# Optimization experiments

Measured on AMD Instinct MI355X. Metric: run time of the kernel, lower is better.

The kernel has to match this reference:

```python
import jax, jax.numpy as jnp
import numpy as np

EPS = 1e-5

def _bn(x, gamma, beta):
    # training-mode BatchNorm1d over (batch, points) per channel; x: [B, C, N]
    mean = x.mean(axis=(0, 2), keepdims=True)
    var = x.var(axis=(0, 2), keepdims=True)
    return gamma[None, :, None] * (x - mean) * jax.lax.rsqrt(var + EPS) + beta[None, :, None]

def _conv_nn(x, idx, W, b):
    # x: [B, Cin, N_in]; idx: [N_out, k]; W: [Cout, Cin, k]
    g = x[:, :, idx]  # gather -> [B, Cin, N_out, k]
    return jnp.einsum('bink,oik->bon', g, W) + b[None, :, None]

def setup_inputs() -> dict:
    key = jax.random.key(0)
    ks = jax.random.split(key, 8)
    B, Cin, Cout = 32, 32, 64
    Nin, Nout, K, KP = 32768, 8192, 9, 4
    s = 0.05
    return {
        'x': jax.random.normal(ks[0], (B, Cin, Nin), jnp.float32),
        'W1': jax.random.normal(ks[1], (Cout, Cin, K), jnp.float32) * s,
        'b1': jnp.zeros((Cout,), jnp.float32),
        'W2': jax.random.normal(ks[2], (Cout, Cout, K), jnp.float32) * s,
        'b2': jnp.zeros((Cout,), jnp.float32),
        'We': jax.random.normal(ks[3], (Cout, Cin), jnp.float32) * s,
        'be': jnp.zeros((Cout,), jnp.float32),
        'g1': jnp.ones((Cout,), jnp.float32), 'beta1': jnp.zeros((Cout,), jnp.float32),
        'g2': jnp.ones((Cout,), jnp.float32), 'beta2': jnp.zeros((Cout,), jnp.float32),
        'g3': jnp.ones((Cout,), jnp.float32), 'beta3': jnp.zeros((Cout,), jnp.float32),
        'idx1': jax.random.randint(ks[4], (Nout, K), 0, Nin, jnp.int32),
        'idx2': jax.random.randint(ks[5], (Nout, K), 0, Nout, jnp.int32),
        'pool_idx': jax.random.randint(ks[6], (Nout, KP), 0, Nin, jnp.int32),
    }

def reference(x, W1, b1, W2, b2, We, be, g1, beta1, g2, beta2, g3, beta3, idx1, idx2, pool_idx):
    # main branch: ConvNN -> BN -> ReLU -> ConvNN -> BN
    out = jax.nn.relu(_bn(_conv_nn(x, idx1, W1, b1), g1, beta1))
    out = _bn(_conv_nn(out, idx2, W2, b2), g2, beta2)
    # shortcut: AvgPoolNN (k=4) -> 1x1 conv expand -> BN
    pooled = x[:, :, pool_idx].mean(axis=-1)  # [B, Cin, N_out]
    identity = _bn(jnp.einsum('bin,oi->bon', pooled, We) + be[None, :, None], g3, beta3)
    return jax.nn.relu(out + identity)
```

## Files before the change

### kernel.cpp

```cpp
#include <hip/hip_runtime.h>
#include <hip/hip_bf16.h>

typedef __attribute__((ext_vector_type(8))) short short8_t;
typedef __attribute__((ext_vector_type(4))) float f32x4_t;

#define NOUT 8192
#define NIN 32768
#define MTOT 262144.0f
#define ST_STRIPES 64

#define MF(a,b,c) __builtin_amdgcn_mfma_f32_16x16x32_bf16((a),(b),(c),0,0,0)

static __device__ __forceinline__ float bf2f(ushort u) {
    union { float f; unsigned int i; } x; x.i = ((unsigned int)u) << 16; return x.f;
}
static __device__ __forceinline__ ushort f2bfx(float f) {
    union { __hip_bfloat16 h; ushort u; } v;
    v.h = __float2bfloat16(f);
    return v.u;
}
static __device__ __forceinline__ short8_t i4s8(int4 v) {
    union { int4 i; short8_t s; } u; u.i = v; return u.s;
}

__global__ __launch_bounds__(256) void transpose_x_kernel(
    const float* __restrict__ x, ushort* __restrict__ xt)
{
    __shared__ ushort T[64][66];
    const int tid = threadIdx.x;
    const int n0 = blockIdx.x * 64, c0 = blockIdx.y * 64;
    const int lane64 = tid & 63, rb = (tid >> 6) * 16;
    #pragma unroll
    for (int r = 0; r < 16; ++r) {
        int c_l = rb + r;
        T[c_l][lane64] = f2bfx(x[(size_t)(c0 + c_l) * NIN + n0 + lane64]);
    }
    __syncthreads();
    #pragma unroll
    for (int r = 0; r < 16; ++r) {
        int n_l = rb + r;
        xt[(size_t)(n0 + n_l) * 1024 + c0 + lane64] = T[lane64][n_l];
    }
}

__global__ __launch_bounds__(256) void prep_w_kernel(
    const float* __restrict__ W1, const float* __restrict__ W2,
    const float* __restrict__ We,
    ushort* __restrict__ w1p, ushort* __restrict__ w2p, ushort* __restrict__ wep,
    float* __restrict__ stz)
{
    int t = blockIdx.x * 256 + threadIdx.x;
    const int N1 = 18432, N2 = 36864, N3 = 2048;
    if (t < 3 * ST_STRIPES * 128) stz[t] = 0.f;
    if (t < N1) {
        int e = t & 7, o = (t >> 3) & 63, seg = t >> 9;
        int fcg = seg & 3, k = seg >> 2;
        int i = fcg * 8 + e;
        w1p[t] = f2bfx(W1[o * 288 + i * 9 + k]);
    } else if (t < N1 + N2) {
        int t2 = t - N1;
        int e = t2 & 7, o = (t2 >> 3) & 63, seg = t2 >> 9;
        int fcg = seg & 3, kk = (seg >> 2) & 1, k = seg >> 3;
        int ci = kk * 32 + fcg * 8 + e;
        w2p[t2] = f2bfx(W2[o * 576 + ci * 9 + k]);
    } else if (t < N1 + N2 + N3) {
        int t3 = t - N1 - N2;
        wep[t3] = f2bfx(We[t3]);
    }
}

__global__ __launch_bounds__(512) void conv1_kernel(
    const ushort* __restrict__ xt, const int* __restrict__ idx1,
    const ushort* __restrict__ w1p, ushort* __restrict__ out1,
    float* __restrict__ st)
{
    __shared__ __align__(16) ushort Wl[18432];
    __shared__ float Ls[128];
    const int tid = threadIdx.x;
    const int lane = tid & 63, wv = tid >> 6;
    const int n = __builtin_amdgcn_readfirstlane(blockIdx.x * 8 + wv);
    const int l15 = lane & 15, fcg = lane >> 4, fc = fcg * 8;

    for (int i = tid; i < 2304; i += 512)
        ((int4*)Wl)[i] = ((const int4*)w1p)[i];
    if (tid < 128) Ls[tid] = 0.f;

    int rows[9];
    {
        const int* idxn = idx1 + n * 9;
        #pragma unroll
        for (int t = 0; t < 9; ++t) rows[t] = idxn[t];
    }
    __syncthreads();

    f32x4_t acc[2][4];
    #pragma unroll
    for (int m = 0; m < 2; ++m)
        #pragma unroll
        for (int nt = 0; nt < 4; ++nt) acc[m][nt] = (f32x4_t){0.f, 0.f, 0.f, 0.f};

    int4 A0[2], A1[2];

#define C1_PRE(K, A) { \
    const ushort* rp = xt + (size_t)rows[K] * 1024 + l15 * 32 + fc; \
    A[0] = *(const int4*)rp;           \
    A[1] = *(const int4*)(rp + 512);   }

#define C1_BODY(K, A) { \
    const ushort* wp = Wl + ((K) * 4 + fcg) * 512; \
    short8_t b0 = *(const short8_t*)(wp + l15 * 8); \
    short8_t b1 = *(const short8_t*)(wp + (16 + l15) * 8); \
    short8_t b2 = *(const short8_t*)(wp + (32 + l15) * 8); \
    short8_t b3 = *(const short8_t*)(wp + (48 + l15) * 8); \
    short8_t af0 = i4s8(A[0]), af1 = i4s8(A[1]); \
    acc[0][0] = MF(af0, b0, acc[0][0]); acc[1][0] = MF(af1, b0, acc[1][0]); \
    acc[0][1] = MF(af0, b1, acc[0][1]); acc[1][1] = MF(af1, b1, acc[1][1]); \
    acc[0][2] = MF(af0, b2, acc[0][2]); acc[1][2] = MF(af1, b2, acc[1][2]); \
    acc[0][3] = MF(af0, b3, acc[0][3]); acc[1][3] = MF(af1, b3, acc[1][3]); }

    C1_PRE(0, A0);
    #pragma unroll
    for (int t = 0; t < 4; ++t) {
        C1_PRE(2 * t + 1, A1);
        C1_BODY(2 * t, A0);
        C1_PRE(2 * t + 2, A0);
        C1_BODY(2 * t + 1, A1);
    }
    C1_BODY(8, A0);
#undef C1_PRE
#undef C1_BODY

    const size_t outbase = (size_t)n * 2048;
    #pragma unroll
    for (int m = 0; m < 2; ++m)
        #pragma unroll
        for (int nt = 0; nt < 4; ++nt)
            #pragma unroll
            for (int j = 0; j < 4; ++j) {
                int b = m * 16 + (lane >> 4) * 4 + j;
                int o = nt * 16 + l15;
                out1[outbase + b * 64 + o] = f2bfx(acc[m][nt][j]);
            }
    #pragma unroll
    for (int nt = 0; nt < 4; ++nt) {
        float s = 0.f, q = 0.f;
        #pragma unroll
        for (int m = 0; m < 2; ++m)
            #pragma unroll
            for (int j = 0; j < 4; ++j) { float v = acc[m][nt][j]; s += v; q += v * v; }
        s += __shfl_xor(s, 16); s += __shfl_xor(s, 32);
        q += __shfl_xor(q, 16); q += __shfl_xor(q, 32);
        if (lane < 16) {
            atomicAdd(&Ls[nt * 16 + lane], s);
            atomicAdd(&Ls[64 + nt * 16 + lane], q);
        }
    }
    __syncthreads();
    if (tid < 128) atomicAdd(&st[(blockIdx.x & (ST_STRIPES - 1)) * 128 + tid], Ls[tid]);
}

__global__ __launch_bounds__(256) void bn_relu_ip_kernel(
    ushort* __restrict__ buf, const float* __restrict__ ac)
{
    const int tid = threadIdx.x;
    const int o0 = (tid * 8) & 63;
    float a[8], c[8];
    #pragma unroll
    for (int e = 0; e < 8; ++e) { a[e] = ac[o0 + e]; c[e] = ac[64 + o0 + e]; }
    size_t base = (size_t)(blockIdx.x * 256 + tid) * 8;
    const size_t stride = (size_t)1024 * 256 * 8;
    for (int it = 0; it < 8; ++it, base += stride) {
        int4 v = *(int4*)(buf + base);
        ushort* pv = (ushort*)&v;
        #pragma unroll
        for (int e = 0; e < 8; ++e)
            pv[e] = f2bfx(fmaxf(a[e] * bf2f(pv[e]) + c[e], 0.f));
        *(int4*)(buf + base) = v;
    }
}

__global__ __launch_bounds__(512) void conv2_kernel(
    const ushort* __restrict__ out1n, const int* __restrict__ idx2,
    const ushort* __restrict__ w2p, ushort* __restrict__ out2,
    float* __restrict__ st)
{
    __shared__ __align__(16) ushort Wl[36864];
    __shared__ float Ls[128];
    const int tid = threadIdx.x;
    const int lane = tid & 63, wv = tid >> 6;
    const int n = __builtin_amdgcn_readfirstlane(blockIdx.x * 8 + wv);
    const int l15 = lane & 15, fcg = lane >> 4, fc = fcg * 8;

    for (int i = tid; i < 4608; i += 512)
        ((int4*)Wl)[i] = ((const int4*)w2p)[i];
    if (tid < 128) Ls[tid] = 0.f;

    int rows[9];
    {
        const int* idxn = idx2 + n * 9;
        #pragma unroll
        for (int t = 0; t < 9; ++t) rows[t] = idxn[t];
    }
    __syncthreads();

    f32x4_t acc[2][4];
    #pragma unroll
    for (int m = 0; m < 2; ++m)
        #pragma unroll
        for (int nt = 0; nt < 4; ++nt) acc[m][nt] = (f32x4_t){0.f, 0.f, 0.f, 0.f};

    int4 A0[4], A1[4];

#define C2_PRE(K, A) { \
    const ushort* rp = out1n + (size_t)rows[K] * 2048 + l15 * 64 + fc; \
    A[0] = *(const int4*)rp;           \
    A[1] = *(const int4*)(rp + 32);    \
    A[2] = *(const int4*)(rp + 1024);  \
    A[3] = *(const int4*)(rp + 1056);  }

#define C2_BODY(K, A) { \
    const ushort* wp0 = Wl + ((K) * 8 + fcg) * 512;         \
    const ushort* wp1 = wp0 + 4 * 512;                       \
    short8_t b00 = *(const short8_t*)(wp0 + l15 * 8); \
    short8_t b10 = *(const short8_t*)(wp0 + (16 + l15) * 8); \
    short8_t b20 = *(const short8_t*)(wp0 + (32 + l15) * 8); \
    short8_t b30 = *(const short8_t*)(wp0 + (48 + l15) * 8); \
    short8_t b01 = *(const short8_t*)(wp1 + l15 * 8); \
    short8_t b11 = *(const short8_t*)(wp1 + (16 + l15) * 8); \
    short8_t b21 = *(const short8_t*)(wp1 + (32 + l15) * 8); \
    short8_t b31 = *(const short8_t*)(wp1 + (48 + l15) * 8); \
    short8_t af00 = i4s8(A[0]), af01 = i4s8(A[1]); \
    short8_t af10 = i4s8(A[2]), af11 = i4s8(A[3]); \
    acc[0][0] = MF(af00, b00, acc[0][0]); acc[0][0] = MF(af01, b01, acc[0][0]); \
    acc[0][1] = MF(af00, b10, acc[0][1]); acc[0][1] = MF(af01, b11, acc[0][1]); \
    acc[0][2] = MF(af00, b20, acc[0][2]); acc[0][2] = MF(af01, b21, acc[0][2]); \
    acc[0][3] = MF(af00, b30, acc[0][3]); acc[0][3] = MF(af01, b31, acc[0][3]); \
    acc[1][0] = MF(af10, b00, acc[1][0]); acc[1][0] = MF(af11, b01, acc[1][0]); \
    acc[1][1] = MF(af10, b10, acc[1][1]); acc[1][1] = MF(af11, b11, acc[1][1]); \
    acc[1][2] = MF(af10, b20, acc[1][2]); acc[1][2] = MF(af11, b21, acc[1][2]); \
    acc[1][3] = MF(af10, b30, acc[1][3]); acc[1][3] = MF(af11, b31, acc[1][3]); }

    C2_PRE(0, A0);
    #pragma unroll
    for (int t = 0; t < 4; ++t) {
        C2_PRE(2 * t + 1, A1);
        C2_BODY(2 * t, A0);
        C2_PRE(2 * t + 2, A0);
        C2_BODY(2 * t + 1, A1);
    }
    C2_BODY(8, A0);
#undef C2_PRE
#undef C2_BODY

    const size_t outbase = (size_t)n * 2048;
    #pragma unroll
    for (int m = 0; m < 2; ++m)
        #pragma unroll
        for (int nt = 0; nt < 4; ++nt)
            #pragma unroll
            for (int j = 0; j < 4; ++j) {
                int b = m * 16 + (lane >> 4) * 4 + j;
                int o = nt * 16 + l15;
                out2[outbase + b * 64 + o] = f2bfx(acc[m][nt][j]);
            }
    #pragma unroll
    for (int nt = 0; nt < 4; ++nt) {
        float s = 0.f, q = 0.f;
        #pragma unroll
        for (int m = 0; m < 2; ++m)
            #pragma unroll
            for (int j = 0; j < 4; ++j) { float v = acc[m][nt][j]; s += v; q += v * v; }
        s += __shfl_xor(s, 16); s += __shfl_xor(s, 32);
        q += __shfl_xor(q, 16); q += __shfl_xor(q, 32);
        if (lane < 16) {
            atomicAdd(&Ls[nt * 16 + lane], s);
            atomicAdd(&Ls[64 + nt * 16 + lane], q);
        }
    }
    __syncthreads();
    if (tid < 128) atomicAdd(&st[(blockIdx.x & (ST_STRIPES - 1)) * 128 + tid], Ls[tid]);
}

__global__ __launch_bounds__(256) void ident_kernel(
    const ushort* __restrict__ xt, const int* __restrict__ pool_idx,
    const ushort* __restrict__ wep, ushort* __restrict__ identt,
    float* __restrict__ st)
{
    __shared__ float Ls[128];
    const int tid = threadIdx.x;
    const int lane = tid & 63, wv = tid >> 6;
    const int n = __builtin_amdgcn_readfirstlane(blockIdx.x * 4 + wv);
    const int l15 = lane & 15, fc = (lane >> 4) * 8;

    const ushort* wpf = wep + l15 * 32 + fc;
    short8_t bfr[4];
    #pragma unroll
    for (int nt = 0; nt < 4; ++nt)
        bfr[nt] = *(const short8_t*)(wpf + nt * 512);

    int prow[4];
    {
        const int* pn = pool_idx + n * 4;
        #pragma unroll
        for (int t = 0; t < 4; ++t) prow[t] = pn[t];
    }
    if (tid < 128) Ls[tid] = 0.f;

    float s0[8], s1[8];
    #pragma unroll
    for (int e = 0; e < 8; ++e) { s0[e] = 0.f; s1[e] = 0.f; }
    #pragma unroll
    for (int kp = 0; kp < 4; ++kp) {
        const ushort* rp = xt + (size_t)prow[kp] * 1024 + l15 * 32 + fc;
        int4 v0 = *(const int4*)rp;
        int4 v1 = *(const int4*)(rp + 512);
        const ushort* p0 = (const ushort*)&v0;
        const ushort* p1 = (const ushort*)&v1;
        #pragma unroll
        for (int e = 0; e < 8; ++e) { s0[e] += bf2f(p0[e]); s1[e] += bf2f(p1[e]); }
    }
    short8_t af0, af1;
    {
        int4 v0, v1; ushort* p0 = (ushort*)&v0; ushort* p1 = (ushort*)&v1;
        #pragma unroll
        for (int e = 0; e < 8; ++e) {
            p0[e] = f2bfx(s0[e] * 0.25f);
            p1[e] = f2bfx(s1[e] * 0.25f);
        }
        af0 = i4s8(v0); af1 = i4s8(v1);
    }

    f32x4_t acc[2][4];
    #pragma unroll
    for (int nt = 0; nt < 4; ++nt) {
        acc[0][nt] = (f32x4_t){0.f, 0.f, 0.f, 0.f};
        acc[1][nt] = (f32x4_t){0.f, 0.f, 0.f, 0.f};
        acc[0][nt] = MF(af0, bfr[nt], acc[0][nt]);
        acc[1][nt] = MF(af1, bfr[nt], acc[1][nt]);
    }

    const size_t outbase = (size_t)n * 2048;
    #pragma unroll
    for (int m = 0; m < 2; ++m)
        #pragma unroll
        for (int nt = 0; nt < 4; ++nt)
            #pragma unroll
            for (int j = 0; j < 4; ++j) {
                int b = m * 16 + (lane >> 4) * 4 + j;
                int o = nt * 16 + l15;
                identt[outbase + b * 64 + o] = f2bfx(acc[m][nt][j]);
            }
    #pragma unroll
    for (int nt = 0; nt < 4; ++nt) {
        float s = 0.f, q = 0.f;
        #pragma unroll
        for (int m = 0; m < 2; ++m)
            #pragma unroll
            for (int j = 0; j < 4; ++j) { float v = acc[m][nt][j]; s += v; q += v * v; }
        s += __shfl_xor(s, 16); s += __shfl_xor(s, 32);
        q += __shfl_xor(q, 16); q += __shfl_xor(q, 32);
        if (lane < 16) {
            atomicAdd(&Ls[nt * 16 + lane], s);
            atomicAdd(&Ls[64 + nt * 16 + lane], q);
        }
    }
    __syncthreads();
    if (tid < 128) atomicAdd(&st[(blockIdx.x & (ST_STRIPES - 1)) * 128 + tid], Ls[tid]);
}

__global__ void finalize_kernel(const float* __restrict__ st, const float* __restrict__ g,
                                const float* __restrict__ bet, float* __restrict__ ac)
{
    int o = threadIdx.x;
    if (o >= 64) return;
    float s = 0.f, q = 0.f;
    for (int i = 0; i < ST_STRIPES; ++i) { s += st[i * 128 + o]; q += st[i * 128 + 64 + o]; }
    float mean = s * (1.0f / MTOT);
    float var  = q * (1.0f / MTOT) - mean * mean;
    float a = g[o] * rsqrtf(var + 1e-5f);
    ac[o] = a;
    ac[64 + o] = bet[o] - a * mean;
}

__global__ void finalize23_kernel(
    const float* __restrict__ st2, const float* __restrict__ g2, const float* __restrict__ b2,
    const float* __restrict__ st3, const float* __restrict__ g3, const float* __restrict__ b3,
    float* __restrict__ ac2, float* __restrict__ ac3)
{
    int o = threadIdx.x;
    if (o >= 64) return;
    const float* st = blockIdx.x ? st3 : st2;
    const float* g  = blockIdx.x ? g3  : g2;
    const float* bt = blockIdx.x ? b3  : b2;
    float* ac       = blockIdx.x ? ac3 : ac2;
    float s = 0.f, q = 0.f;
    for (int i = 0; i < ST_STRIPES; ++i) { s += st[i * 128 + o]; q += st[i * 128 + 64 + o]; }
    float mean = s * (1.0f / MTOT);
    float var  = q * (1.0f / MTOT) - mean * mean;
    float a = g[o] * rsqrtf(var + 1e-5f);
    ac[o] = a;
    ac[64 + o] = bt[o] - a * mean;
}

__global__ __launch_bounds__(256) void final_combine_kernel(
    const ushort* __restrict__ out2, const ushort* __restrict__ idt,
    const float* __restrict__ ac2, const float* __restrict__ ac3,
    float* __restrict__ dout)
{
    __shared__ float tile[64][65];
    const int tid = threadIdx.x;
    const int n0 = blockIdx.x * 64, bo0 = blockIdx.y * 64;
    const int lane64 = tid & 63, rb = (tid >> 6) * 16;
    const int o = lane64;
    const float a2 = ac2[o], c2 = ac2[64 + o], a3 = ac3[o], c3 = ac3[64 + o];
    #pragma unroll
    for (int r = 0; r < 16; ++r) {
        int n_l = rb + r;
        size_t p = (size_t)(n0 + n_l) * 2048 + bo0 + lane64;
        float v = a2 * bf2f(out2[p]) + c2 + a3 * bf2f(idt[p]) + c3;
        tile[n_l][lane64] = fmaxf(v, 0.f);
    }
    __syncthreads();
    #pragma unroll
    for (int r = 0; r < 16; ++r) {
        int bo_l = rb + r;
        dout[(size_t)(bo0 + bo_l) * NOUT + n0 + lane64] = tile[lane64][bo_l];
    }
}

extern "C" void kernel_launch(void* const* d_in, const int* in_sizes, int n_in,
                              void* d_out, int out_size, void* d_ws, size_t ws_size,
                              hipStream_t stream)
{
    const float* x     = (const float*)d_in[0];
    const float* W1    = (const float*)d_in[1];
    const float* W2    = (const float*)d_in[3];
    const float* We    = (const float*)d_in[5];
    const float* g1    = (const float*)d_in[7];
    const float* beta1 = (const float*)d_in[8];
    const float* g2    = (const float*)d_in[9];
    const float* beta2 = (const float*)d_in[10];
    const float* g3    = (const float*)d_in[11];
    const float* beta3 = (const float*)d_in[12];
    const int* idx1    = (const int*)d_in[13];
    const int* idx2    = (const int*)d_in[14];
    const int* pool_idx= (const int*)d_in[15];
    float* dout = (float*)d_out;

    char* ws = (char*)d_ws;
    const size_t off_xt   = 0;
    const size_t off_out1 = 67108864;
    const size_t off_out2 = 100663296;
    const size_t off_id   = 134217728;
    const size_t off_w1p  = 167772160;
    const size_t off_w2p  = 167809024;
    const size_t off_wep  = 167882752;
    const size_t off_st   = 167886848;
    const size_t off_ac   = 167985152;
    const size_t need     = 167986688;
    if (ws_size < need) return;

    ushort* xt   = (ushort*)(ws + off_xt);
    ushort* out1 = (ushort*)(ws + off_out1);
    ushort* out2 = (ushort*)(ws + off_out2);
    ushort* idt  = (ushort*)(ws + off_id);
    ushort* w1p  = (ushort*)(ws + off_w1p);
    ushort* w2p  = (ushort*)(ws + off_w2p);
    ushort* wep  = (ushort*)(ws + off_wep);
    float*  st1  = (float*)(ws + off_st);
    float*  st2  = st1 + 64 * 128;
    float*  st3  = st1 + 2 * 64 * 128;
    float*  ac1  = (float*)(ws + off_ac);
    float*  ac2  = ac1 + 128;
    float*  ac3  = ac1 + 256;

    prep_w_kernel<<<224, 256, 0, stream>>>(W1, W2, We, w1p, w2p, wep, st1);
    transpose_x_kernel<<<dim3(512, 16), 256, 0, stream>>>(x, xt);
    conv1_kernel<<<1024, 512, 0, stream>>>(xt, idx1, w1p, out1, st1);
    ident_kernel<<<2048, 256, 0, stream>>>(xt, pool_idx, wep, idt, st3);
    finalize_kernel<<<1, 64, 0, stream>>>(st1, g1, beta1, ac1);
    bn_relu_ip_kernel<<<1024, 256, 0, stream>>>(out1, ac1);
    conv2_kernel<<<1024, 512, 0, stream>>>(out1, idx2, w2p, out2, st2);
    finalize23_kernel<<<2, 64, 0, stream>>>(st2, g2, beta2, st3, g3, beta3, ac2, ac3);
    final_combine_kernel<<<dim3(128, 32), 256, 0, stream>>>(out2, idt, ac2, ac3, dout);
}
```

Measured before the change: 191.2 us.

## Fuse BN1+ReLU into conv2 gather and deepen load prefetch pipelines

Removes the separate in-place BN+ReLU pass over out1 and applies the per-channel scale/shift and ReLU to the gathered rows inside conv2. This avoids a full read and write of the 32MB intermediate. Each gathered row is used by about 9 neighbours, so the BN math is repeated roughly 9 times per element. Both conv kernels also prefetch 3-4 gathered rows ahead instead of 1 and get a launch_bounds occupancy hint, which raises register pressure.

```diff
diff --git a/kernel.cpp b/kernel.cpp
--- a/kernel.cpp
+++ b/kernel.cpp
@@ -21,6 +21,14 @@
 }
 static __device__ __forceinline__ short8_t i4s8(int4 v) {
     union { int4 i; short8_t s; } u; u.i = v; return u.s;
+}
+
+static __device__ __forceinline__ short8_t bn8(int4 v, const float* a8, const float* c8) {
+    ushort* pv = (ushort*)&v;
+    #pragma unroll
+    for (int e = 0; e < 8; ++e)
+        pv[e] = f2bfx(fmaxf(a8[e] * bf2f(pv[e]) + c8[e], 0.f));
+    return i4s8(v);
 }
 
 __global__ __launch_bounds__(256) void transpose_x_kernel(
@@ -69,7 +77,7 @@
     }
 }
 
-__global__ __launch_bounds__(512) void conv1_kernel(
+__global__ __launch_bounds__(512, 4) void conv1_kernel(
     const ushort* __restrict__ xt, const int* __restrict__ idx1,
     const ushort* __restrict__ w1p, ushort* __restrict__ out1,
     float* __restrict__ st)
@@ -99,7 +107,7 @@
         #pragma unroll
         for (int nt = 0; nt < 4; ++nt) acc[m][nt] = (f32x4_t){0.f, 0.f, 0.f, 0.f};
 
-    int4 A0[2], A1[2];
+    int4 A0[2], A1[2], A2[2], A3[2];
 
 #define C1_PRE(K, A) { \
     const ushort* rp = xt + (size_t)rows[K] * 1024 + l15 * 32 + fc; \
@@ -118,14 +126,15 @@
     acc[0][2] = MF(af0, b2, acc[0][2]); acc[1][2] = MF(af1, b2, acc[1][2]); \
     acc[0][3] = MF(af0, b3, acc[0][3]); acc[1][3] = MF(af1, b3, acc[1][3]); }
 
-    C1_PRE(0, A0);
-    #pragma unroll
-    for (int t = 0; t < 4; ++t) {
-        C1_PRE(2 * t + 1, A1);
-        C1_BODY(2 * t, A0);
-        C1_PRE(2 * t + 2, A0);
-        C1_BODY(2 * t + 1, A1);
-    }
+    C1_PRE(0, A0); C1_PRE(1, A1); C1_PRE(2, A2); C1_PRE(3, A3);
+    C1_BODY(0, A0); C1_PRE(4, A0);
+    C1_BODY(1, A1); C1_PRE(5, A1);
+    C1_BODY(2, A2); C1_PRE(6, A2);
+    C1_BODY(3, A3); C1_PRE(7, A3);
+    C1_BODY(4, A0); C1_PRE(8, A0);
+    C1_BODY(5, A1);
+    C1_BODY(6, A2);
+    C1_BODY(7, A3);
     C1_BODY(8, A0);
 #undef C1_PRE
 #undef C1_BODY
@@ -159,30 +168,10 @@
     if (tid < 128) atomicAdd(&st[(blockIdx.x & (ST_STRIPES - 1)) * 128 + tid], Ls[tid]);
 }
 
-__global__ __launch_bounds__(256) void bn_relu_ip_kernel(
-    ushort* __restrict__ buf, const float* __restrict__ ac)
-{
-    const int tid = threadIdx.x;
-    const int o0 = (tid * 8) & 63;
-    float a[8], c[8];
-    #pragma unroll
-    for (int e = 0; e < 8; ++e) { a[e] = ac[o0 + e]; c[e] = ac[64 + o0 + e]; }
-    size_t base = (size_t)(blockIdx.x * 256 + tid) * 8;
-    const size_t stride = (size_t)1024 * 256 * 8;
-    for (int it = 0; it < 8; ++it, base += stride) {
-        int4 v = *(int4*)(buf + base);
-        ushort* pv = (ushort*)&v;
-        #pragma unroll
-        for (int e = 0; e < 8; ++e)
-            pv[e] = f2bfx(fmaxf(a[e] * bf2f(pv[e]) + c[e], 0.f));
-        *(int4*)(buf + base) = v;
-    }
-}
-
-__global__ __launch_bounds__(512) void conv2_kernel(
-    const ushort* __restrict__ out1n, const int* __restrict__ idx2,
-    const ushort* __restrict__ w2p, ushort* __restrict__ out2,
-    float* __restrict__ st)
+__global__ __launch_bounds__(512, 4) void conv2_kernel(
+    const ushort* __restrict__ out1raw, const int* __restrict__ idx2,
+    const ushort* __restrict__ w2p, const float* __restrict__ ac1,
+    ushort* __restrict__ out2, float* __restrict__ st)
 {
     __shared__ __align__(16) ushort Wl[36864];
     __shared__ float Ls[128];
@@ -201,6 +190,12 @@
         #pragma unroll
         for (int t = 0; t < 9; ++t) rows[t] = idxn[t];
     }
+    float a0r[8], c0r[8], a1r[8], c1r[8];
+    #pragma unroll
+    for (int e = 0; e < 8; ++e) {
+        a0r[e] = ac1[fc + e];       c0r[e] = ac1[64 + fc + e];
+        a1r[e] = ac1[32 + fc + e];  c1r[e] = ac1[96 + fc + e];
+    }
     __syncthreads();
 
     f32x4_t acc[2][4];
@@ -209,10 +204,10 @@
         #pragma unroll
         for (int nt = 0; nt < 4; ++nt) acc[m][nt] = (f32x4_t){0.f, 0.f, 0.f, 0.f};
 
-    int4 A0[4], A1[4];
+    int4 A0[4], A1[4], A2[4];
 
 #define C2_PRE(K, A) { \
-    const ushort* rp = out1n + (size_t)rows[K] * 2048 + l15 * 64 + fc; \
+    const ushort* rp = out1raw + (size_t)rows[K] * 2048 + l15 * 64 + fc; \
     A[0] = *(const int4*)rp;           \
     A[1] = *(const int4*)(rp + 32);    \
     A[2] = *(const int4*)(rp + 1024);  \
@@ -229,8 +224,10 @@
     short8_t b11 = *(const short8_t*)(wp1 + (16 + l15) * 8); \
     short8_t b21 = *(const short8_t*)(wp1 + (32 + l15) * 8); \
     short8_t b31 = *(const short8_t*)(wp1 + (48 + l15) * 8); \
-    short8_t af00 = i4s8(A[0]), af01 = i4s8(A[1]); \
-    short8_t af10 = i4s8(A[2]), af11 = i4s8(A[3]); \
+    short8_t af00 = bn8(A[0], a0r, c0r); \
+    short8_t af01 = bn8(A[1], a1r, c1r); \
+    short8_t af10 = bn8(A[2], a0r, c0r); \
+    short8_t af11 = bn8(A[3], a1r, c1r); \
     acc[0][0] = MF(af00, b00, acc[0][0]); acc[0][0] = MF(af01, b01, acc[0][0]); \
     acc[0][1] = MF(af00, b10, acc[0][1]); acc[0][1] = MF(af01, b11, acc[0][1]); \
     acc[0][2] = MF(af00, b20, acc[0][2]); acc[0][2] = MF(af01, b21, acc[0][2]); \
@@ -240,15 +237,16 @@
     acc[1][2] = MF(af10, b20, acc[1][2]); acc[1][2] = MF(af11, b21, acc[1][2]); \
     acc[1][3] = MF(af10, b30, acc[1][3]); acc[1][3] = MF(af11, b31, acc[1][3]); }
 
-    C2_PRE(0, A0);
-    #pragma unroll
-    for (int t = 0; t < 4; ++t) {
-        C2_PRE(2 * t + 1, A1);
-        C2_BODY(2 * t, A0);
-        C2_PRE(2 * t + 2, A0);
-        C2_BODY(2 * t + 1, A1);
-    }
-    C2_BODY(8, A0);
+    C2_PRE(0, A0); C2_PRE(1, A1); C2_PRE(2, A2);
+    C2_BODY(0, A0); C2_PRE(3, A0);
+    C2_BODY(1, A1); C2_PRE(4, A1);
+    C2_BODY(2, A2); C2_PRE(5, A2);
+    C2_BODY(3, A0); C2_PRE(6, A0);
+    C2_BODY(4, A1); C2_PRE(7, A1);
+    C2_BODY(5, A2); C2_PRE(8, A2);
+    C2_BODY(6, A0);
+    C2_BODY(7, A1);
+    C2_BODY(8, A2);
 #undef C2_PRE
 #undef C2_BODY
 
@@ -479,8 +477,7 @@
     conv1_kernel<<<1024, 512, 0, stream>>>(xt, idx1, w1p, out1, st1);
     ident_kernel<<<2048, 256, 0, stream>>>(xt, pool_idx, wep, idt, st3);
     finalize_kernel<<<1, 64, 0, stream>>>(st1, g1, beta1, ac1);
-    bn_relu_ip_kernel<<<1024, 256, 0, stream>>>(out1, ac1);
-    conv2_kernel<<<1024, 512, 0, stream>>>(out1, idx2, w2p, out2, st2);
+    conv2_kernel<<<1024, 512, 0, stream>>>(out1, idx2, w2p, ac1, out2, st2);
     finalize23_kernel<<<2, 64, 0, stream>>>(st2, g2, beta2, st3, g3, beta3, ac2, ac3);
     final_combine_kernel<<<dim3(128, 32), 256, 0, stream>>>(out2, idt, ac2, ac3, dout);
 }
```

New measurement: 180.1 us. 5.8% less time.
